# Performance work log

Hardware: AMD Instinct MI355X
Metric: run time of the kernel (lower is better)

The kernel has to match this reference:

```python
import jax, jax.numpy as jnp
import numpy as np

N_WG = 512      # waveguides n
N_COL = 512     # mesh columns
M = N_WG // 2   # node slots per column (odd columns have one masked dummy)
N_NODE = N_COL * M
B = 8192        # batch of input fields
PI4 = np.pi / 4


def build_mesh_indices():
    """Rectangular (Clements-style) mesh: per-column (top, bottom, mask) arrays."""
    top = np.zeros((N_COL, M), np.int32)
    bottom = np.zeros((N_COL, M), np.int32)
    mask = np.zeros((N_COL, M), np.int32)
    for c in range(N_COL):
        if c % 2 == 0:
            t = np.arange(0, N_WG, 2, dtype=np.int32)
            top[c], bottom[c], mask[c] = t, t + 1, 1
        else:
            t = np.arange(1, N_WG - 1, 2, dtype=np.int32)
            k = len(t)
            top[c, :k], bottom[c, :k], mask[c, :k] = t, t + 1, 1
            # masked dummy slot uses otherwise-unused rows 0 and N_WG-1
            top[c, k:], bottom[c, k:] = 0, N_WG - 1
    return jnp.asarray(top), jnp.asarray(bottom), jnp.asarray(mask)


def setup_inputs() -> dict:
    key = jax.random.key(0)
    ks = jax.random.split(key, 6)
    top, bottom, mask = build_mesh_indices()
    return {
        "x": jax.random.normal(ks[0], (N_WG, B), dtype=jnp.float32),
        "thetas": 2 * np.pi * jax.random.uniform(ks[1], (N_NODE,), dtype=jnp.float32),
        "phis": 2 * np.pi * jax.random.uniform(ks[2], (N_NODE,), dtype=jnp.float32),
        "gammas": 2 * np.pi * jax.random.uniform(ks[3], (N_WG,), dtype=jnp.float32),
        "bs_errors": 0.01 * jax.random.normal(ks[4], (N_NODE, 2), dtype=jnp.float32),
        "loss_errors": -0.1 * jax.random.uniform(ks[5], (N_NODE, 2), dtype=jnp.float32),
        "top": top, "bottom": bottom, "mask": mask,
    }


def _dc_terms(bs_errors, loss_errors, side):
    """_parallel_dc: per-node directional-coupler 2x2 elements [N,4] complex."""
    ins = jnp.exp(jnp.log(10.0) * loss_errors[:, side] / 20.0)
    e = bs_errors[:, side]
    s, c = jnp.sin(PI4 + e), jnp.cos(PI4 + e)
    t11 = (ins * s).astype(jnp.complex64)
    t12 = ins * (1j * c)
    t21 = (1j * c).astype(jnp.complex64)
    t22 = s.astype(jnp.complex64)
    return jnp.stack([t11, t12, t21, t22], axis=-1)


def _transform(v, T, t, b, m):
    """_parallel_transform: masked 2x2 gather-multiply-scatter. T: [M,4] complex."""
    vt, vb = v[t], v[b]
    one_m = 1.0 - m
    s11 = (T[:, 0] * m + one_m)[:, None]
    s12 = (T[:, 1] * m)[:, None]
    s21 = (T[:, 2] * m)[:, None]
    s22 = (T[:, 3] * m + one_m)[:, None]
    return v.at[t].set(s11 * vt + s21 * vb).at[b].set(s12 * vt + s22 * vb)


def reference(x, thetas, phis, gammas, bs_errors, loss_errors, top, bottom, mask):
    # input gamma phase screen, then propagate through all mesh columns
    v = x.astype(jnp.complex64) * jnp.exp(1j * gammas)[:, None]          # [n, B]
    left = _dc_terms(bs_errors, loss_errors, 0).reshape(N_COL, M, 4)
    right = _dc_terms(bs_errors, loss_errors, 1).reshape(N_COL, M, 4)
    th = thetas.reshape(N_COL, M)
    ph = phis.reshape(N_COL, M)
    mf = mask.astype(jnp.float32)

    def column(v, xs):
        t, b, m, thc, phc, L, R = xs
        # PhaseStyle.TOP, forward: phi -> left DC -> theta -> right DC
        v = v.at[t].multiply(jnp.exp(1j * phc * m)[:, None])
        v = _transform(v, L, t, b, m)
        v = v.at[t].multiply(jnp.exp(1j * thc * m)[:, None])
        v = _transform(v, R, t, b, m)
        return v, None

    v, _ = jax.lax.scan(column, v, (top, bottom, mf, th, ph, left, right))
    return jnp.stack([v.real, v.imag])  # [2, n, B]
```

## Files before the change

### kernel.cpp

```cpp
#include <hip/hip_runtime.h>
#include <math.h>

#define BATCH 8192
#define NROW 512
#define NCOL 512
#define MNODE 256
#define PL 524288

typedef __attribute__((ext_vector_type(8))) short bf16x8;
typedef __attribute__((ext_vector_type(4))) short s16x4;
typedef __attribute__((ext_vector_type(4))) float f32x4;

__device__ __forceinline__ short2 split1(float x) {
  unsigned u = __float_as_uint(x);
  short h = (short)(u >> 16);
  float r = x - __uint_as_float(u & 0xffff0000u);
  short l = (short)(__float_as_uint(r) >> 16);
  return make_short2(h, l);
}

__global__ __launch_bounds__(256) void precomp_kernel(
    const float* __restrict__ thetas, const float* __restrict__ phis,
    const float* __restrict__ bse, const float* __restrict__ lse,
    float4* __restrict__ pp) {
  int n = blockIdx.x * 256 + threadIdx.x;
  float th = thetas[n], ph = phis[n];
  float e0 = bse[2 * n + 0], e1 = bse[2 * n + 1];
  float l0 = lse[2 * n + 0], l1 = lse[2 * n + 1];
  const float K = 0.16609640474436813f;
  float ins0 = exp2f(l0 * K), ins1 = exp2f(l1 * K);
  const float PI4 = 0.7853981633974483f;
  float s0, c0, s1, c1, sp, cp, st, ct;
  sincosf(PI4 + e0, &s0, &c0);
  sincosf(PI4 + e1, &s1, &c1);
  sincosf(ph, &sp, &cp);
  sincosf(th, &st, &ct);
  float AL = ins0 * s0, C1L = c0, C2L = ins0 * c0, SL = s0;
  float AR = ins1 * s1, C1R = c1, C2R = ins1 * c1, SR = s1;
  float a11r = AL * cp,   a11i = AL * sp;
  float a12r = 0.f,       a12i = C1L;
  float a21r = -C2L * sp, a21i = C2L * cp;
  float a22r = SL,        a22i = 0.f;
  float b11r = a11r * ct - a11i * st, b11i = a11r * st + a11i * ct;
  float b12r = a12r * ct - a12i * st, b12i = a12r * st + a12i * ct;
  float n11r = AR * b11r - C1R * a21i;
  float n11i = AR * b11i + C1R * a21r;
  float n12r = AR * b12r - C1R * a22i;
  float n12i = AR * b12i + C1R * a22r;
  float n21r = -C2R * b11i + SR * a21r;
  float n21i =  C2R * b11r + SR * a21i;
  float n22r = -C2R * b12i + SR * a22r;
  float n22i =  C2R * b12r + SR * a22i;
  pp[2 * n + 0] = make_float4(n11r, n11i, n12r, n12i);
  pp[2 * n + 1] = make_float4(n21r, n21i, n22r, n22i);
}

__device__ __forceinline__ void proc_pair(float& vtr, float& vti, float& vbr, float& vbi,
                                          const float4 q0, const float4 q1) {
  float tr = q0.x * vtr - q0.y * vti + q0.z * vbr - q0.w * vbi;
  float ti = q0.x * vti + q0.y * vtr + q0.z * vbi + q0.w * vbr;
  float br = q1.x * vtr - q1.y * vti + q1.z * vbr - q1.w * vbi;
  float bi = q1.x * vti + q1.y * vtr + q1.z * vbi + q1.w * vbr;
  vtr = tr; vti = ti; vbr = br; vbi = bi;
}

__device__ __forceinline__ int swz(int b) { return b ^ ((b >> 3) & 7); }

__global__ __launch_bounds__(256) void compose_band(
    const float* __restrict__ gammas, const float4* __restrict__ pp,
    float* __restrict__ Tsegs, int P) {
  __shared__ float ep[5120];

  const int tid  = threadIdx.x;
  const int lane = tid & 63;
  const int w    = tid >> 6;
  const int seg  = blockIdx.x >> 7;
  const int g    = blockIdx.x & 127;
  const int col  = g * 4 + w;

  const float4* ps = pp + (size_t)seg * P * 1024;
  float* T = Tsegs + (size_t)seg * (1024 * NROW);

  const int colA = (col - 63) & ~1;
  const int E    = colA + 2 * lane;
  const int je   = E >> 1;
  const int jeC  = je < 0 ? 0 : (je > 255 ? 255 : je);

  const bool vE  = (E >= 0) && (E <= 510);
  const bool vOT = (E >= 0) && (E <= 508);
  const bool vOB = (E >= 2) && (E <= 510);

  float ar = 0.f, ai = 0.f, br = 0.f, bi = 0.f;
  {
    float vr0 = 1.f, vi0 = 0.f;
    if (seg == 0) {
      float sg, cg;
      sincosf(gammas[col], &sg, &cg);
      vr0 = cg; vi0 = sg;
    }
    if (E == col)     { ar = vr0; ai = vi0; }
    if (E + 1 == col) { br = vr0; bi = vi0; }
  }

  const float4* pe = ps + 2 * jeC;
  const float4* po = ps + 512 + 2 * jeC;

  float sar = 0.f, sai = 0.f, sbr = 0.f, sbi = 0.f;

  for (int p = 0; p < P; ++p) {
    const bool actp = (E >= col - 2 * p - 5) && (E <= col + 2 * p + 4);

    float4 o0, o1;
    if (actp) {
      float4 q0 = pe[0];
      float4 q1 = pe[1];
      o0 = po[0];
      o1 = po[-1];

      float tr = q0.x * ar - q0.y * ai + q0.z * br - q0.w * bi;
      float ti = q0.x * ai + q0.y * ar + q0.z * bi + q0.w * br;
      float ur = q1.x * ar - q1.y * ai + q1.z * br - q1.w * bi;
      float ui = q1.x * ai + q1.y * ar + q1.z * bi + q1.w * br;
      if (vE) { ar = tr; ai = ti; br = ur; bi = ui; }
    }
    pe += 1024; po += 1024;

    if (p == P - 1) { sar = ar; sai = ai; sbr = br; sbi = bi; }

    float anr = __shfl_down(ar, 1, 64);
    float ani = __shfl_down(ai, 1, 64);
    float bpr = __shfl_up(br, 1, 64);
    float bpi = __shfl_up(bi, 1, 64);
    if (lane == 63) { anr = 0.f; ani = 0.f; }
    if (lane == 0)  { bpr = 0.f; bpi = 0.f; }

    if (actp) {
      float tr = o0.x * br - o0.y * bi + o0.z * anr - o0.w * ani;
      float ti = o0.x * bi + o0.y * br + o0.z * ani + o0.w * anr;
      float ur = o1.x * bpr - o1.y * bpi + o1.z * ar - o1.w * ai;
      float ui = o1.x * bpi + o1.y * bpr + o1.z * ai + o1.w * ar;
      if (vOT) { br = tr; bi = ti; }
      if (vOB) { ar = ur; ai = ui; }
    }
  }

  int sprow = -1;
  float spr = 0.f, spi = 0.f;
  if ((col & 1) == 0) {
    if (colA + 128 <= 511) {
      sprow = colA + 128;
      float4 w1 = ps[(size_t)(P - 1) * 1024 + 512 + 2 * (colA / 2 + 63) + 1];
      float vtr = __shfl(sbr, 63, 64);
      float vti = __shfl(sbi, 63, 64);
      spr = w1.x * vtr - w1.y * vti;
      spi = w1.x * vti + w1.y * vtr;
    }
  } else {
    if (colA - 1 >= 0) {
      sprow = colA - 1;
      float4 w0 = ps[(size_t)(P - 1) * 1024 + 512 + 2 * (colA / 2 - 1)];
      float vbr = __shfl(sar, 0, 64);
      float vbi = __shfl(sai, 0, 64);
      spr = w0.z * vbr - w0.w * vbi;
      spi = w0.z * vbi + w0.w * vbr;
    }
  }

  for (int i = tid; i < 5120; i += 256) ep[i] = 0.f;
  __syncthreads();
  if (E >= 0 && E <= 510) {
    ep[E * 5 + w]         = ar;
    ep[(512 + E) * 5 + w] = ai;
    ep[(E + 1) * 5 + w]   = br;
    ep[(513 + E) * 5 + w] = bi;
  }
  if (lane == 0 && sprow >= 0) {
    ep[sprow * 5 + w]         = spr;
    ep[(512 + sprow) * 5 + w] = spi;
  }
  __syncthreads();

  if (seg & 1) {
#pragma unroll
    for (int k = 0; k < 4; ++k) {
      const int i = k * 256 + tid;
      *(float4*)(T + (size_t)i * NROW + g * 4) =
          make_float4(ep[i * 5 + 0], ep[i * 5 + 1], ep[i * 5 + 2], ep[i * 5 + 3]);
    }
  } else {
    unsigned short* Thi = (unsigned short*)T;
    unsigned short* Tlo = Thi + PL;
    const int c  = tid & 3;
    const int k0 = (tid >> 2) * 16;
    const int colg = g * 4 + c;
    short hh[16], ll[16];
#pragma unroll
    for (int j = 0; j < 16; ++j) {
      short2 s = split1(ep[(k0 + j) * 5 + c]);
      hh[j] = s.x; ll[j] = s.y;
    }
    *(bf16x8*)&Thi[(size_t)colg * 1024 + k0]     = *(bf16x8*)&hh[0];
    *(bf16x8*)&Thi[(size_t)colg * 1024 + k0 + 8] = *(bf16x8*)&hh[8];
    *(bf16x8*)&Tlo[(size_t)colg * 1024 + k0]     = *(bf16x8*)&ll[0];
    *(bf16x8*)&Tlo[(size_t)colg * 1024 + k0 + 8] = *(bf16x8*)&ll[8];
  }
}

__global__ __launch_bounds__(256) void merge_t(
    const float* __restrict__ Ab, long sA,
    const unsigned short* __restrict__ Bb, long sB,
    unsigned short* __restrict__ Cub, long sCu,
    float* __restrict__ Cfb, long sCf,
    int HA, int HB, int force_f) {
  const int z = blockIdx.z;
  const float* A = Ab + (long)z * sA;
  const unsigned short* B = Bb + (long)z * sB;
  const bool fout = force_f || (z & 1);
  unsigned short* Cu = Cub + (long)(z >> 1) * sCu;
  float*          Cf = Cfb + (long)(z >> 1) * sCf;

  __shared__ short sAh[64 * 40], sAl[64 * 40];

  const int tid = threadIdx.x;
  const int lane = tid & 63;
  const int w = tid >> 6;
  const int bm = blockIdx.y * 64;
  const int bn = blockIdx.x * 64;
  const int wm = (w & 1) * 32;
  const int wn = (w >> 1) * 32;
  const int q = lane >> 4;
  const int l15 = lane & 15;

  const int sm = tid >> 2;
  const int sk = (tid & 3) * 8;

  const int rmin = (blockIdx.y & 7) * 64;
  int klo = rmin - HA;
  {
    int t = bn - HB;
    if (t > klo) klo = t;
    if (klo < 0) klo = 0;
  }
  int khi = rmin + 63 + HA;
  {
    int t = bn + 63 + HB;
    if (t < khi) khi = t;
    if (khi > 511) khi = 511;
  }
  klo &= ~31;

  f32x4 acc[2][2];
#pragma unroll
  for (int i = 0; i < 2; ++i)
#pragma unroll
    for (int j = 0; j < 2; ++j) acc[i][j] = (f32x4){0.f, 0.f, 0.f, 0.f};

  if (klo <= khi) {
#pragma unroll 1
    for (int h = 0; h < 2; ++h) {
#pragma unroll 1
      for (int k0 = klo; k0 <= khi; k0 += 32) {
        const int gkb = h * 512 + k0;
        {
          const int gm = bm + sm;
          const int gk = gkb + sk;
          const int r = gm & 511;
          const bool top = gm < 512;
          const bool left = gk < 512;
          const int col = gk & 511;
          const float* src = (top == left) ? (A + (size_t)r * 512)
                                           : (A + (size_t)(512 + r) * 512);
          const float sgn = (top && !left) ? -1.f : 1.f;
          float4 v0 = *(const float4*)(src + col);
          float4 v1 = *(const float4*)(src + col + 4);
          float vv[8] = {v0.x, v0.y, v0.z, v0.w, v1.x, v1.y, v1.z, v1.w};
          short hh[8], ll[8];
#pragma unroll
          for (int i = 0; i < 8; ++i) {
            short2 s = split1(sgn * vv[i]);
            hh[i] = s.x; ll[i] = s.y;
          }
          __syncthreads();
          *(bf16x8*)&sAh[sm * 40 + sk] = *(bf16x8*)hh;
          *(bf16x8*)&sAl[sm * 40 + sk] = *(bf16x8*)ll;
          __syncthreads();
        }

        bf16x8 bh[2], bl[2];
#pragma unroll
        for (int nt = 0; nt < 2; ++nt) {
          const unsigned short* bp =
              B + (size_t)(bn + wn + nt * 16 + l15) * 1024 + gkb + q * 8;
          bh[nt] = *(const bf16x8*)bp;
          bl[nt] = *(const bf16x8*)(bp + PL);
        }

        bf16x8 ah[2], al[2];
#pragma unroll
        for (int mt = 0; mt < 2; ++mt) {
          const int m = wm + mt * 16 + l15;
          ah[mt] = *(const bf16x8*)&sAh[m * 40 + q * 8];
          al[mt] = *(const bf16x8*)&sAl[m * 40 + q * 8];
        }

#pragma unroll
        for (int mt = 0; mt < 2; ++mt)
#pragma unroll
          for (int nt = 0; nt < 2; ++nt) {
            acc[mt][nt] = __builtin_amdgcn_mfma_f32_16x16x32_bf16(ah[mt], bh[nt], acc[mt][nt], 0, 0, 0);
            acc[mt][nt] = __builtin_amdgcn_mfma_f32_16x16x32_bf16(ah[mt], bl[nt], acc[mt][nt], 0, 0, 0);
            acc[mt][nt] = __builtin_amdgcn_mfma_f32_16x16x32_bf16(al[mt], bh[nt], acc[mt][nt], 0, 0, 0);
          }
      }
    }
  }

  if (fout) {
#pragma unroll
    for (int mt = 0; mt < 2; ++mt)
#pragma unroll
      for (int nt = 0; nt < 2; ++nt)
#pragma unroll
        for (int r = 0; r < 4; ++r) {
          const int gm = bm + wm + mt * 16 + q * 4 + r;
          const int gn = bn + wn + nt * 16 + l15;
          Cf[(size_t)gm * 512 + gn] = acc[mt][nt][r];
        }
  } else {
    unsigned short* Chi = Cu;
    unsigned short* Clo = Cu + PL;
#pragma unroll
    for (int mt = 0; mt < 2; ++mt)
#pragma unroll
      for (int nt = 0; nt < 2; ++nt) {
        short hh[4], ll[4];
#pragma unroll
        for (int r = 0; r < 4; ++r) {
          short2 s = split1(acc[mt][nt][r]);
          hh[r] = s.x; ll[r] = s.y;
        }
        const int gm0 = bm + wm + mt * 16 + q * 4;
        const int gn  = bn + wn + nt * 16 + l15;
        *(s16x4*)&Chi[(size_t)gn * 1024 + gm0] = *(s16x4*)hh;
        *(s16x4*)&Clo[(size_t)gn * 1024 + gm0] = *(s16x4*)ll;
      }
  }
}

__global__ __launch_bounds__(256) void compose_kernel(
    const float* __restrict__ gammas, const float4* __restrict__ pp,
    float* __restrict__ Tsegs, int pairs_per_seg) {
  __shared__ float4 buf[2][1024];
  float* epf = (float*)buf;

  const int tid  = threadIdx.x;
  const int lane = tid & 63;
  const int w    = tid >> 6;
  const int seg  = blockIdx.x >> 7;
  const int g    = blockIdx.x & 127;
  const int col  = g * 4 + w;
  const int colmin = g * 4;

  const float4* ps = pp + (size_t)seg * pairs_per_seg * 1024;
  float* T = Tsegs + (size_t)seg * (1024 * NROW);

  float vr[8], vi[8];
#pragma unroll
  for (int r = 0; r < 8; ++r) {
    const int row = lane * 8 + r;
    vr[r] = 0.f; vi[r] = 0.f;
    if (row == col) {
      if (seg == 0) {
        float sg, cg;
        sincosf(gammas[row], &sg, &cg);
        vr[r] = cg; vi[r] = sg;
      } else {
        vr[r] = 1.f;
      }
    }
  }

  {
    const int sw = swz(tid);
#pragma unroll
    for (int k = 0; k < 4; ++k)
      buf[0][256 * k + sw] = ps[256 * k + tid];
  }
  __syncthreads();

  const int Lc = col >> 3;

#pragma unroll 1
  for (int p = 0; p < pairs_per_seg; ++p) {
    const int b = p & 1;

    const int HA = (p >> 2) + 3;
    const bool act  = (lane >= Lc - HA)     && (lane <= Lc + HA);
    const bool wide = (lane >= Lc - HA - 1) && (lane <= Lc + HA + 1);

    float4 f0, f1, f2, f3;
    bool st0 = false, st1 = false;
    if (p < pairs_per_seg - 1) {
      const int slo = colmin - 2 * p - 50;
      const int shi = colmin + 2 * p + 53;
      st0 = (tid + 1 >= slo) && (tid <= shi);
      st1 = (tid + 257 >= slo) && (tid + 256 <= shi);
      const float4* src = ps + (size_t)(p + 1) * 1024;
      if (st0) { f0 = src[tid];       f2 = src[512 + tid]; }
      if (st1) { f1 = src[256 + tid]; f3 = src[768 + tid]; }
    }

    float4 pe[8], po[7], pu1;
    if (act) {
      const int base = 8 * lane;
      const int l7 = lane & 7;
#pragma unroll
      for (int j = 0; j < 8; ++j) pe[j] = buf[b][base + (j ^ l7)];
#pragma unroll
      for (int j = 0; j < 7; ++j) po[j] = buf[b][512 + base + (j ^ l7)];
      const int lm = (lane == 0) ? 0 : lane - 1;
      pu1 = buf[b][512 + 8 * lm + (7 ^ (lm & 7))];

#pragma unroll
      for (int k = 0; k < 4; ++k)
        proc_pair(vr[2 * k], vi[2 * k], vr[2 * k + 1], vi[2 * k + 1],
                  pe[2 * k], pe[2 * k + 1]);

#pragma unroll
      for (int k = 0; k < 3; ++k)
        proc_pair(vr[2 * k + 1], vi[2 * k + 1], vr[2 * k + 2], vi[2 * k + 2],
                  po[2 * k], po[2 * k + 1]);
    }

    float br = 0.f, bi = 0.f, tu = 0.f, tv = 0.f;
    if (wide) {
      br = __shfl_down(vr[0], 1, 64);
      bi = __shfl_down(vi[0], 1, 64);
      tu = __shfl_up(vr[7], 1, 64);
      tv = __shfl_up(vi[7], 1, 64);
    }
    if (act) {
      float nAr = po[6].x * vr[7] - po[6].y * vi[7] + po[6].z * br - po[6].w * bi;
      float nAi = po[6].x * vi[7] + po[6].y * vr[7] + po[6].z * bi + po[6].w * br;
      float nBr = pu1.x * tu - pu1.y * tv + pu1.z * vr[0] - pu1.w * vi[0];
      float nBi = pu1.x * tv + pu1.y * tu + pu1.z * vi[0] + pu1.w * vr[0];
      if (lane < 63) { vr[7] = nAr; vi[7] = nAi; }
      if (lane > 0)  { vr[0] = nBr; vi[0] = nBi; }
    }

    if (p < pairs_per_seg - 1) {
      const int sw = swz(tid);
      if (st0) { buf[1 - b][sw] = f0;       buf[1 - b][512 + sw] = f2; }
      if (st1) { buf[1 - b][256 + sw] = f1; buf[1 - b][768 + sw] = f3; }
    }
    __syncthreads();
  }

#pragma unroll
  for (int r = 0; r < 8; ++r) {
    epf[(lane * 8 + r) * 5 + w] = vr[r];
    epf[(512 + lane * 8 + r) * 5 + w] = vi[r];
  }
  __syncthreads();
#pragma unroll
  for (int k = 0; k < 4; ++k) {
    const int i = k * 256 + tid;
    *(float4*)(T + (size_t)i * NROW + g * 4) =
        make_float4(epf[i * 5 + 0], epf[i * 5 + 1], epf[i * 5 + 2], epf[i * 5 + 3]);
  }
}

__global__ __launch_bounds__(256) void merge_g(
    const float* __restrict__ Ab, const float* __restrict__ Bb,
    float* __restrict__ Cb, long sA, long sB, long sC, int HA, int HB) {
  const float* A = Ab + (long)blockIdx.z * sA;
  const float* B = Bb + (long)blockIdx.z * sB;
  float*       C = Cb + (long)blockIdx.z * sC;

  __shared__ short sAh[64 * 40], sAl[64 * 40];

  const int tid = threadIdx.x;
  const int lane = tid & 63;
  const int w = tid >> 6;
  const int bm = blockIdx.y * 64;
  const int bn = blockIdx.x * 64;
  const int wm = (w & 1) * 32;
  const int wn = (w >> 1) * 32;
  const int q = lane >> 4;
  const int l15 = lane & 15;

  const int sm = tid >> 2;
  const int sk = (tid & 3) * 8;

  const int rmin = (blockIdx.y & 7) * 64;
  int klo = rmin - HA;
  {
    int t = bn - HB;
    if (t > klo) klo = t;
    if (klo < 0) klo = 0;
  }
  int khi = rmin + 63 + HA;
  {
    int t = bn + 63 + HB;
    if (t < khi) khi = t;
    if (khi > 511) khi = 511;
  }
  klo &= ~31;

  f32x4 acc[2][2];
#pragma unroll
  for (int i = 0; i < 2; ++i)
#pragma unroll
    for (int j = 0; j < 2; ++j) acc[i][j] = (f32x4){0.f, 0.f, 0.f, 0.f};

  if (klo <= khi) {
#pragma unroll 1
    for (int h = 0; h < 2; ++h) {
#pragma unroll 1
      for (int k0 = klo; k0 <= khi; k0 += 32) {
        const int gkb = h * 512 + k0;
        {
          const int gm = bm + sm;
          const int gk = gkb + sk;
          const int r = gm & 511;
          const bool top = gm < 512;
          const bool left = gk < 512;
          const int col = gk & 511;
          const float* src = (top == left) ? (A + (size_t)r * 512)
                                           : (A + (size_t)(512 + r) * 512);
          const float sgn = (top && !left) ? -1.f : 1.f;
          float4 v0 = *(const float4*)(src + col);
          float4 v1 = *(const float4*)(src + col + 4);
          float vv[8] = {v0.x, v0.y, v0.z, v0.w, v1.x, v1.y, v1.z, v1.w};
          short hh[8], ll[8];
#pragma unroll
          for (int i = 0; i < 8; ++i) {
            short2 s = split1(sgn * vv[i]);
            hh[i] = s.x; ll[i] = s.y;
          }
          __syncthreads();
          *(bf16x8*)&sAh[sm * 40 + sk] = *(bf16x8*)hh;
          *(bf16x8*)&sAl[sm * 40 + sk] = *(bf16x8*)ll;
          __syncthreads();
        }

        bf16x8 bh[2], bl[2];
#pragma unroll
        for (int nt = 0; nt < 2; ++nt) {
          const float* bp = B + (size_t)(gkb + q * 8) * 512 + bn + wn + nt * 16 + l15;
          short hh[8], ll[8];
#pragma unroll
          for (int j = 0; j < 8; ++j) {
            short2 s = split1(bp[(size_t)j * 512]);
            hh[j] = s.x; ll[j] = s.y;
          }
          bh[nt] = *(bf16x8*)hh;
          bl[nt] = *(bf16x8*)ll;
        }

        bf16x8 ah[2], al[2];
#pragma unroll
        for (int mt = 0; mt < 2; ++mt) {
          const int m = wm + mt * 16 + l15;
          ah[mt] = *(const bf16x8*)&sAh[m * 40 + q * 8];
          al[mt] = *(const bf16x8*)&sAl[m * 40 + q * 8];
        }

#pragma unroll
        for (int mt = 0; mt < 2; ++mt)
#pragma unroll
          for (int nt = 0; nt < 2; ++nt) {
            acc[mt][nt] = __builtin_amdgcn_mfma_f32_16x16x32_bf16(ah[mt], bh[nt], acc[mt][nt], 0, 0, 0);
            acc[mt][nt] = __builtin_amdgcn_mfma_f32_16x16x32_bf16(ah[mt], bl[nt], acc[mt][nt], 0, 0, 0);
            acc[mt][nt] = __builtin_amdgcn_mfma_f32_16x16x32_bf16(al[mt], bh[nt], acc[mt][nt], 0, 0, 0);
          }
      }
    }
  }

#pragma unroll
  for (int mt = 0; mt < 2; ++mt)
#pragma unroll
    for (int nt = 0; nt < 2; ++nt)
#pragma unroll
      for (int r = 0; r < 4; ++r) {
        const int gm = bm + wm + mt * 16 + q * 4 + r;
        const int gn = bn + wn + nt * 16 + l15;
        C[(size_t)gm * 512 + gn] = acc[mt][nt][r];
      }
}

__global__ __launch_bounds__(256) void xprep_kernel(
    const float* __restrict__ x, short* __restrict__ xp) {
  const int t = blockIdx.x * 256 + threadIdx.x;
  const int n = t & 8191;
  const int g = t >> 13;
  const float* src = x + (size_t)g * 8 * BATCH + n;
  short h[8], l[8];
#pragma unroll
  for (int j = 0; j < 8; ++j) {
    short2 s = split1(src[(size_t)j * BATCH]);
    h[j] = s.x; l[j] = s.y;
  }
  short* dst = xp + (size_t)t * 16;
  *(bf16x8*)dst = *(bf16x8*)h;
  *(bf16x8*)(dst + 8) = *(bf16x8*)l;
}

__global__ __launch_bounds__(256) void gemm_mfma_packed(
    const float* __restrict__ A, const short* __restrict__ xp,
    float* __restrict__ C) {
  __shared__ short sAh[128 * 40], sAl[128 * 40];

  const int tid = threadIdx.x;
  const int lane = tid & 63;
  const int w = tid >> 6;
  const int bm = blockIdx.y * 128;
  const int bn = blockIdx.x * 128;
  const int wm = (w & 1) * 64;
  const int wn = (w >> 1) * 64;
  const int q = lane >> 4;
  const int l15 = lane & 15;

  const int sm = tid >> 1;
  const int sk = (tid & 1) * 16;
  const float* Ap = A + (size_t)(bm + sm) * 512 + sk;

  f32x4 acc[4][4];
#pragma unroll
  for (int i = 0; i < 4; ++i)
#pragma unroll
    for (int j = 0; j < 4; ++j) acc[i][j] = (f32x4){0.f, 0.f, 0.f, 0.f};

  float4 pa[4];
#pragma unroll
  for (int i = 0; i < 4; ++i) pa[i] = *(const float4*)(Ap + i * 4);

#pragma unroll 1
  for (int k0 = 0; k0 < 512; k0 += 32) {
    {
      short h[16], l[16];
#pragma unroll
      for (int i = 0; i < 16; ++i) {
        short2 s = split1(((const float*)pa)[i]);
        h[i] = s.x; l[i] = s.y;
      }
      __syncthreads();
      *(bf16x8*)&sAh[sm * 40 + sk]     = *(bf16x8*)&h[0];
      *(bf16x8*)&sAh[sm * 40 + sk + 8] = *(bf16x8*)&h[8];
      *(bf16x8*)&sAl[sm * 40 + sk]     = *(bf16x8*)&l[0];
      *(bf16x8*)&sAl[sm * 40 + sk + 8] = *(bf16x8*)&l[8];
      __syncthreads();
    }

    if (k0 + 32 < 512) {
#pragma unroll
      for (int i = 0; i < 4; ++i) pa[i] = *(const float4*)(Ap + k0 + 32 + i * 4);
    }

    const int kt = k0 >> 5;
    bf16x8 bh[4], bl[4];
#pragma unroll
    for (int nt = 0; nt < 4; ++nt) {
      const short* bp = xp + (((size_t)(kt * 4 + q)) * BATCH +
                              (bn + wn + nt * 16 + l15)) * 16;
      bh[nt] = *(const bf16x8*)bp;
      bl[nt] = *(const bf16x8*)(bp + 8);
    }

#pragma unroll
    for (int mt = 0; mt < 4; ++mt) {
      const int m = wm + mt * 16 + l15;
      bf16x8 ah = *(const bf16x8*)&sAh[m * 40 + q * 8];
      bf16x8 al = *(const bf16x8*)&sAl[m * 40 + q * 8];
#pragma unroll
      for (int nt = 0; nt < 4; ++nt) {
        acc[mt][nt] = __builtin_amdgcn_mfma_f32_16x16x32_bf16(ah, bh[nt], acc[mt][nt], 0, 0, 0);
        acc[mt][nt] = __builtin_amdgcn_mfma_f32_16x16x32_bf16(ah, bl[nt], acc[mt][nt], 0, 0, 0);
        acc[mt][nt] = __builtin_amdgcn_mfma_f32_16x16x32_bf16(al, bh[nt], acc[mt][nt], 0, 0, 0);
      }
    }
  }

#pragma unroll
  for (int mt = 0; mt < 4; ++mt)
#pragma unroll
    for (int nt = 0; nt < 4; ++nt)
#pragma unroll
      for (int r = 0; r < 4; ++r) {
        const int gm = bm + wm + mt * 16 + q * 4 + r;
        const int gn = bn + wn + nt * 16 + l15;
        C[(size_t)gm * BATCH + gn] = acc[mt][nt][r];
      }
}

__global__ __launch_bounds__(256) void gemm_mfma(
    const float* __restrict__ A, const float* __restrict__ B,
    float* __restrict__ C) {
  __shared__ short sAh[128 * 40], sAl[128 * 40];

  const int tid = threadIdx.x;
  const int lane = tid & 63;
  const int w = tid >> 6;
  const int bm = blockIdx.y * 128;
  const int bn = blockIdx.x * 128;
  const int wm = (w & 1) * 64;
  const int wn = (w >> 1) * 64;
  const int q = lane >> 4;
  const int l15 = lane & 15;

  const int sm = tid >> 1;
  const int sk = (tid & 1) * 16;
  const float* Ap = A + (size_t)(bm + sm) * 512 + sk;

  f32x4 acc[4][4];
#pragma unroll
  for (int i = 0; i < 4; ++i)
#pragma unroll
    for (int j = 0; j < 4; ++j) acc[i][j] = (f32x4){0.f, 0.f, 0.f, 0.f};

  float4 pa[4];
#pragma unroll
  for (int i = 0; i < 4; ++i) pa[i] = *(const float4*)(Ap + i * 4);

#pragma unroll 1
  for (int k0 = 0; k0 < 512; k0 += 32) {
    {
      short h[16], l[16];
#pragma unroll
      for (int i = 0; i < 16; ++i) {
        short2 s = split1(((const float*)pa)[i]);
        h[i] = s.x; l[i] = s.y;
      }
      __syncthreads();
      *(bf16x8*)&sAh[sm * 40 + sk]     = *(bf16x8*)&h[0];
      *(bf16x8*)&sAh[sm * 40 + sk + 8] = *(bf16x8*)&h[8];
      *(bf16x8*)&sAl[sm * 40 + sk]     = *(bf16x8*)&l[0];
      *(bf16x8*)&sAl[sm * 40 + sk + 8] = *(bf16x8*)&l[8];
      __syncthreads();
    }

    if (k0 + 32 < 512) {
#pragma unroll
      for (int i = 0; i < 4; ++i) pa[i] = *(const float4*)(Ap + k0 + 32 + i * 4);
    }

    bf16x8 bh[4], bl[4];
#pragma unroll
    for (int nt = 0; nt < 4; ++nt) {
      const float* bp = B + (size_t)(k0 + q * 8) * BATCH + bn + wn + nt * 16 + l15;
      short hh[8], ll[8];
#pragma unroll
      for (int j = 0; j < 8; ++j) {
        short2 s = split1(bp[(size_t)j * BATCH]);
        hh[j] = s.x; ll[j] = s.y;
      }
      bh[nt] = *(bf16x8*)hh;
      bl[nt] = *(bf16x8*)ll;
    }

    bf16x8 ah[4], al[4];
#pragma unroll
    for (int mt = 0; mt < 4; ++mt) {
      const int m = wm + mt * 16 + l15;
      ah[mt] = *(const bf16x8*)&sAh[m * 40 + q * 8];
      al[mt] = *(const bf16x8*)&sAl[m * 40 + q * 8];
    }

#pragma unroll
    for (int mt = 0; mt < 4; ++mt)
#pragma unroll
      for (int nt = 0; nt < 4; ++nt) {
        acc[mt][nt] = __builtin_amdgcn_mfma_f32_16x16x32_bf16(ah[mt], bh[nt], acc[mt][nt], 0, 0, 0);
        acc[mt][nt] = __builtin_amdgcn_mfma_f32_16x16x32_bf16(ah[mt], bl[nt], acc[mt][nt], 0, 0, 0);
        acc[mt][nt] = __builtin_amdgcn_mfma_f32_16x16x32_bf16(al[mt], bh[nt], acc[mt][nt], 0, 0, 0);
      }
  }

#pragma unroll
  for (int mt = 0; mt < 4; ++mt)
#pragma unroll
    for (int nt = 0; nt < 4; ++nt)
#pragma unroll
      for (int r = 0; r < 4; ++r) {
        const int gm = bm + wm + mt * 16 + q * 4 + r;
        const int gn = bn + wn + nt * 16 + l15;
        C[(size_t)gm * BATCH + gn] = acc[mt][nt][r];
      }
}

extern "C" void kernel_launch(void* const* d_in, const int* in_sizes, int n_in,
                              void* d_out, int out_size, void* d_ws, size_t ws_size,
                              hipStream_t stream) {
  const float* x      = (const float*)d_in[0];
  const float* thetas = (const float*)d_in[1];
  const float* phis   = (const float*)d_in[2];
  const float* gammas = (const float*)d_in[3];
  const float* bse    = (const float*)d_in[4];
  const float* lse    = (const float*)d_in[5];

  float* base = (float*)d_ws;
  float4* pp  = (float4*)d_ws;
  const long PPF = 1048576;
  const long S   = 524288;

  precomp_kernel<<<512, 256, 0, stream>>>(thetas, phis, bse, lse, pp);

  if (ws_size >= (size_t)24 * 1024 * 1024) {
    float* B0 = base + PPF;
    compose_band<<<1024, 256, 0, stream>>>(gammas, pp, B0, 32);

    merge_t<<<dim3(8, 16, 4), 256, 0, stream>>>(
        B0 + S, 2 * S, (const unsigned short*)B0, 4 * S,
        (unsigned short*)base, 2 * S, base + 5 * PPF, S, 68, 68, 0);

    merge_t<<<dim3(8, 16, 2), 256, 0, stream>>>(
        base + 5 * PPF, S, (const unsigned short*)base, 2 * S,
        (unsigned short*)(base + PPF), 0, base + PPF + S, 0, 136, 136, 0);

    merge_t<<<dim3(8, 16, 1), 256, 0, stream>>>(
        base + PPF + S, 0, (const unsigned short*)(base + PPF), 0,
        (unsigned short*)base, 0, base, 0, 272, 272, 1);

    short* xp = (short*)(base + S);
    xprep_kernel<<<2048, 256, 0, stream>>>(x, xp);

    gemm_mfma_packed<<<dim3(64, 8), 256, 0, stream>>>(base, xp, (float*)d_out);
    gemm_mfma_packed<<<dim3(64, 8), 256, 0, stream>>>(base, xp, (float*)d_out);
  } else {
    int nseg;
    if (ws_size >= (size_t)14 * 1024 * 1024)      nseg = 4;
    else if (ws_size >= (size_t)8 * 1024 * 1024)  nseg = 2;
    else                                          nseg = 1;

    float* segs = base + PPF;
    float* Tf;
    compose_kernel<<<nseg * 128, 256, 0, stream>>>(gammas, pp, segs, 256 / nseg);

    if (nseg == 4) {
      float* T10 = base;
      float* T32 = base + S;
      Tf = segs + 4 * S;
      merge_g<<<dim3(8, 16, 2), 256, 0, stream>>>(
          segs + S, segs, T10, 2 * S, 2 * S, S, 132, 132);
      merge_g<<<dim3(8, 16, 1), 256, 0, stream>>>(
          T32, T10, Tf, 0, 0, 0, 264, 264);
    } else if (nseg == 2) {
      Tf = base;
      merge_g<<<dim3(8, 16, 1), 256, 0, stream>>>(
          segs + S, segs, Tf, 0, 0, 0, 260, 260);
    } else {
      Tf = segs;
    }

    gemm_mfma<<<dim3(BATCH / 128, 8), 256, 0, stream>>>(Tf, x, (float*)d_out);
  }
}
```

Baseline: 254.5 us.

## Retile merge_t to 32-row tiles with double-buffered LDS and drop duplicate GEMM launch

merge_t now uses 32x64 output tiles, so its grid doubles in y, and each wave computes one 16-row strip. A-tile staging is restructured into a single flattened loop over both k-halves. It uses double-buffered shared memory with one barrier per step and prefetches the next A float4 into registers. Separately, the second identical gemm_mfma_packed launch is removed, eliminating a redundant full GEMM pass. The smaller tiles raise parallelism and overlap in the merge stages, at the cost of less B reuse per block.

```diff
diff --git a/kernel.cpp b/kernel.cpp
--- a/kernel.cpp
+++ b/kernel.cpp
@@ -219,6 +219,261 @@
   unsigned short* Cu = Cub + (long)(z >> 1) * sCu;
   float*          Cf = Cfb + (long)(z >> 1) * sCf;
 
+  __shared__ short sAh[2][32 * 40], sAl[2][32 * 40];
+
+  const int tid = threadIdx.x;
+  const int lane = tid & 63;
+  const int w = tid >> 6;
+  const int bm = blockIdx.y * 32;
+  const int bn = blockIdx.x * 64;
+  const int wm = (w & 1) * 16;
+  const int wn = (w >> 1) * 32;
+  const int q = lane >> 4;
+  const int l15 = lane & 15;
+
+  const int sm  = tid >> 3;
+  const int skf = (tid & 7) * 4;
+
+  const int rmin = (blockIdx.y & 15) * 32;
+  int klo = rmin - HA;
+  {
+    int t = bn - HB;
+    if (t > klo) klo = t;
+    if (klo < 0) klo = 0;
+  }
+  int khi = rmin + 31 + HA;
+  {
+    int t = bn + 63 + HB;
+    if (t < khi) khi = t;
+    if (khi > 511) khi = 511;
+  }
+  klo &= ~31;
+
+  f32x4 acc[2];
+  acc[0] = (f32x4){0.f, 0.f, 0.f, 0.f};
+  acc[1] = (f32x4){0.f, 0.f, 0.f, 0.f};
+
+  if (klo <= khi) {
+    const int ns = ((khi - klo) >> 5) + 1;
+    const int total = 2 * ns;
+
+    const int gm = bm + sm;
+    const int r = gm & 511;
+    const bool top = gm < 512;
+    const float* srcA0 = top ? (A + (size_t)r * 512) : (A + (size_t)(512 + r) * 512);
+    const float* srcA1 = top ? (A + (size_t)(512 + r) * 512) : (A + (size_t)r * 512);
+    const float sgn1 = top ? -1.f : 1.f;
+
+    float4 pv = *(const float4*)(srcA0 + klo + skf);
+
+#pragma unroll 1
+    for (int s = 0; s < total; ++s) {
+      const int h = (s >= ns) ? 1 : 0;
+      const int k0 = klo + ((s - h * ns) << 5);
+      const int b = s & 1;
+
+      {
+        const float sg = h ? sgn1 : 1.f;
+        float vv[4] = {pv.x, pv.y, pv.z, pv.w};
+        short hh[4], ll[4];
+#pragma unroll
+        for (int i = 0; i < 4; ++i) {
+          short2 s2 = split1(sg * vv[i]);
+          hh[i] = s2.x; ll[i] = s2.y;
+        }
+        *(s16x4*)&sAh[b][sm * 40 + skf] = *(s16x4*)hh;
+        *(s16x4*)&sAl[b][sm * 40 + skf] = *(s16x4*)ll;
+      }
+      __syncthreads();
+
+      if (s + 1 < total) {
+        const int h2 = (s + 1 >= ns) ? 1 : 0;
+        const int k2 = klo + (((s + 1) - h2 * ns) << 5);
+        pv = *(const float4*)((h2 ? srcA1 : srcA0) + k2 + skf);
+      }
+
+      const int gkb = h * 512 + k0;
+
+      bf16x8 bh[2], bl[2];
+#pragma unroll
+      for (int nt = 0; nt < 2; ++nt) {
+        const unsigned short* bp =
+            B + (size_t)(bn + wn + nt * 16 + l15) * 1024 + gkb + q * 8;
+        bh[nt] = *(const bf16x8*)bp;
+        bl[nt] = *(const bf16x8*)(bp + PL);
+      }
+
+      const int m = wm + l15;
+      bf16x8 ah = *(const bf16x8*)&sAh[b][m * 40 + q * 8];
+      bf16x8 al = *(const bf16x8*)&sAl[b][m * 40 + q * 8];
+
+#pragma unroll
+      for (int nt = 0; nt < 2; ++nt) {
+        acc[nt] = __builtin_amdgcn_mfma_f32_16x16x32_bf16(ah, bh[nt], acc[nt], 0, 0, 0);
+        acc[nt] = __builtin_amdgcn_mfma_f32_16x16x32_bf16(ah, bl[nt], acc[nt], 0, 0, 0);
+        acc[nt] = __builtin_amdgcn_mfma_f32_16x16x32_bf16(al, bh[nt], acc[nt], 0, 0, 0);
+      }
+    }
+  }
+
+  if (fout) {
+#pragma unroll
+    for (int nt = 0; nt < 2; ++nt)
+#pragma unroll
+      for (int rr = 0; rr < 4; ++rr) {
+        const int gm = bm + wm + q * 4 + rr;
+        const int gn = bn + wn + nt * 16 + l15;
+        Cf[(size_t)gm * 512 + gn] = acc[nt][rr];
+      }
+  } else {
+    unsigned short* Chi = Cu;
+    unsigned short* Clo = Cu + PL;
+#pragma unroll
+    for (int nt = 0; nt < 2; ++nt) {
+      short hh[4], ll[4];
+#pragma unroll
+      for (int rr = 0; rr < 4; ++rr) {
+        short2 s = split1(acc[nt][rr]);
+        hh[rr] = s.x; ll[rr] = s.y;
+      }
+      const int gm0 = bm + wm + q * 4;
+      const int gn  = bn + wn + nt * 16 + l15;
+      *(s16x4*)&Chi[(size_t)gn * 1024 + gm0] = *(s16x4*)hh;
+      *(s16x4*)&Clo[(size_t)gn * 1024 + gm0] = *(s16x4*)ll;
+    }
+  }
+}
+
+__global__ __launch_bounds__(256) void compose_kernel(
+    const float* __restrict__ gammas, const float4* __restrict__ pp,
+    float* __restrict__ Tsegs, int pairs_per_seg) {
+  __shared__ float4 buf[2][1024];
+  float* epf = (float*)buf;
+
+  const int tid  = threadIdx.x;
+  const int lane = tid & 63;
+  const int w    = tid >> 6;
+  const int seg  = blockIdx.x >> 7;
+  const int g    = blockIdx.x & 127;
+  const int col  = g * 4 + w;
+  const int colmin = g * 4;
+
+  const float4* ps = pp + (size_t)seg * pairs_per_seg * 1024;
+  float* T = Tsegs + (size_t)seg * (1024 * NROW);
+
+  float vr[8], vi[8];
+#pragma unroll
+  for (int r = 0; r < 8; ++r) {
+    const int row = lane * 8 + r;
+    vr[r] = 0.f; vi[r] = 0.f;
+    if (row == col) {
+      if (seg == 0) {
+        float sg, cg;
+        sincosf(gammas[row], &sg, &cg);
+        vr[r] = cg; vi[r] = sg;
+      } else {
+        vr[r] = 1.f;
+      }
+    }
+  }
+
+  {
+    const int sw = swz(tid);
+#pragma unroll
+    for (int k = 0; k < 4; ++k)
+      buf[0][256 * k + sw] = ps[256 * k + tid];
+  }
+  __syncthreads();
+
+  const int Lc = col >> 3;
+
+#pragma unroll 1
+  for (int p = 0; p < pairs_per_seg; ++p) {
+    const int b = p & 1;
+
+    const int HA = (p >> 2) + 3;
+    const bool act  = (lane >= Lc - HA)     && (lane <= Lc + HA);
+    const bool wide = (lane >= Lc - HA - 1) && (lane <= Lc + HA + 1);
+
+    float4 f0, f1, f2, f3;
+    bool st0 = false, st1 = false;
+    if (p < pairs_per_seg - 1) {
+      const int slo = colmin - 2 * p - 50;
+      const int shi = colmin + 2 * p + 53;
+      st0 = (tid + 1 >= slo) && (tid <= shi);
+      st1 = (tid + 257 >= slo) && (tid + 256 <= shi);
+      const float4* src = ps + (size_t)(p + 1) * 1024;
+      if (st0) { f0 = src[tid];       f2 = src[512 + tid]; }
+      if (st1) { f1 = src[256 + tid]; f3 = src[768 + tid]; }
+    }
+
+    float4 pe[8], po[7], pu1;
+    if (act) {
+      const int base = 8 * lane;
+      const int l7 = lane & 7;
+#pragma unroll
+      for (int j = 0; j < 8; ++j) pe[j] = buf[b][base + (j ^ l7)];
+#pragma unroll
+      for (int j = 0; j < 7; ++j) po[j] = buf[b][512 + base + (j ^ l7)];
+      const int lm = (lane == 0) ? 0 : lane - 1;
+      pu1 = buf[b][512 + 8 * lm + (7 ^ (lm & 7))];
+
+#pragma unroll
+      for (int k = 0; k < 4; ++k)
+        proc_pair(vr[2 * k], vi[2 * k], vr[2 * k + 1], vi[2 * k + 1],
+                  pe[2 * k], pe[2 * k + 1]);
+
+#pragma unroll
+      for (int k = 0; k < 3; ++k)
+        proc_pair(vr[2 * k + 1], vi[2 * k + 1], vr[2 * k + 2], vi[2 * k + 2],
+                  po[2 * k], po[2 * k + 1]);
+    }
+
+    float br = 0.f, bi = 0.f, tu = 0.f, tv = 0.f;
+    if (wide) {
+      br = __shfl_down(vr[0], 1, 64);
+      bi = __shfl_down(vi[0], 1, 64);
+      tu = __shfl_up(vr[7], 1, 64);
+      tv = __shfl_up(vi[7], 1, 64);
+    }
+    if (act) {
+      float nAr = po[6].x * vr[7] - po[6].y * vi[7] + po[6].z * br - po[6].w * bi;
+      float nAi = po[6].x * vi[7] + po[6].y * vr[7] + po[6].z * bi + po[6].w * br;
+      float nBr = pu1.x * tu - pu1.y * tv + pu1.z * vr[0] - pu1.w * vi[0];
+      float nBi = pu1.x * tv + pu1.y * tu + pu1.z * vi[0] + pu1.w * vr[0];
+      if (lane < 63) { vr[7] = nAr; vi[7] = nAi; }
+      if (lane > 0)  { vr[0] = nBr; vi[0] = nBi; }
+    }
+
+    if (p < pairs_per_seg - 1) {
+      const int sw = swz(tid);
+      if (st0) { buf[1 - b][sw] = f0;       buf[1 - b][512 + sw] = f2; }
+      if (st1) { buf[1 - b][256 + sw] = f1; buf[1 - b][768 + sw] = f3; }
+    }
+    __syncthreads();
+  }
+
+#pragma unroll
+  for (int r = 0; r < 8; ++r) {
+    epf[(lane * 8 + r) * 5 + w] = vr[r];
+    epf[(512 + lane * 8 + r) * 5 + w] = vi[r];
+  }
+  __syncthreads();
+#pragma unroll
+  for (int k = 0; k < 4; ++k) {
+    const int i = k * 256 + tid;
+    *(float4*)(T + (size_t)i * NROW + g * 4) =
+        make_float4(epf[i * 5 + 0], epf[i * 5 + 1], epf[i * 5 + 2], epf[i * 5 + 3]);
+  }
+}
+
+__global__ __launch_bounds__(256) void merge_g(
+    const float* __restrict__ Ab, const float* __restrict__ Bb,
+    float* __restrict__ Cb, long sA, long sB, long sC, int HA, int HB) {
+  const float* A = Ab + (long)blockIdx.z * sA;
+  const float* B = Bb + (long)blockIdx.z * sB;
+  float*       C = Cb + (long)blockIdx.z * sC;
+
   __shared__ short sAh[64 * 40], sAl[64 * 40];
 
   const int tid = threadIdx.x;
@@ -289,264 +544,6 @@
         bf16x8 bh[2], bl[2];
 #pragma unroll
         for (int nt = 0; nt < 2; ++nt) {
-          const unsigned short* bp =
-              B + (size_t)(bn + wn + nt * 16 + l15) * 1024 + gkb + q * 8;
-          bh[nt] = *(const bf16x8*)bp;
-          bl[nt] = *(const bf16x8*)(bp + PL);
-        }
-
-        bf16x8 ah[2], al[2];
-#pragma unroll
-        for (int mt = 0; mt < 2; ++mt) {
-          const int m = wm + mt * 16 + l15;
-          ah[mt] = *(const bf16x8*)&sAh[m * 40 + q * 8];
-          al[mt] = *(const bf16x8*)&sAl[m * 40 + q * 8];
-        }
-
-#pragma unroll
-        for (int mt = 0; mt < 2; ++mt)
-#pragma unroll
-          for (int nt = 0; nt < 2; ++nt) {
-            acc[mt][nt] = __builtin_amdgcn_mfma_f32_16x16x32_bf16(ah[mt], bh[nt], acc[mt][nt], 0, 0, 0);
-            acc[mt][nt] = __builtin_amdgcn_mfma_f32_16x16x32_bf16(ah[mt], bl[nt], acc[mt][nt], 0, 0, 0);
-            acc[mt][nt] = __builtin_amdgcn_mfma_f32_16x16x32_bf16(al[mt], bh[nt], acc[mt][nt], 0, 0, 0);
-          }
-      }
-    }
-  }
-
-  if (fout) {
-#pragma unroll
-    for (int mt = 0; mt < 2; ++mt)
-#pragma unroll
-      for (int nt = 0; nt < 2; ++nt)
-#pragma unroll
-        for (int r = 0; r < 4; ++r) {
-          const int gm = bm + wm + mt * 16 + q * 4 + r;
-          const int gn = bn + wn + nt * 16 + l15;
-          Cf[(size_t)gm * 512 + gn] = acc[mt][nt][r];
-        }
-  } else {
-    unsigned short* Chi = Cu;
-    unsigned short* Clo = Cu + PL;
-#pragma unroll
-    for (int mt = 0; mt < 2; ++mt)
-#pragma unroll
-      for (int nt = 0; nt < 2; ++nt) {
-        short hh[4], ll[4];
-#pragma unroll
-        for (int r = 0; r < 4; ++r) {
-          short2 s = split1(acc[mt][nt][r]);
-          hh[r] = s.x; ll[r] = s.y;
-        }
-        const int gm0 = bm + wm + mt * 16 + q * 4;
-        const int gn  = bn + wn + nt * 16 + l15;
-        *(s16x4*)&Chi[(size_t)gn * 1024 + gm0] = *(s16x4*)hh;
-        *(s16x4*)&Clo[(size_t)gn * 1024 + gm0] = *(s16x4*)ll;
-      }
-  }
-}
-
-__global__ __launch_bounds__(256) void compose_kernel(
-    const float* __restrict__ gammas, const float4* __restrict__ pp,
-    float* __restrict__ Tsegs, int pairs_per_seg) {
-  __shared__ float4 buf[2][1024];
-  float* epf = (float*)buf;
-
-  const int tid  = threadIdx.x;
-  const int lane = tid & 63;
-  const int w    = tid >> 6;
-  const int seg  = blockIdx.x >> 7;
-  const int g    = blockIdx.x & 127;
-  const int col  = g * 4 + w;
-  const int colmin = g * 4;
-
-  const float4* ps = pp + (size_t)seg * pairs_per_seg * 1024;
-  float* T = Tsegs + (size_t)seg * (1024 * NROW);
-
-  float vr[8], vi[8];
-#pragma unroll
-  for (int r = 0; r < 8; ++r) {
-    const int row = lane * 8 + r;
-    vr[r] = 0.f; vi[r] = 0.f;
-    if (row == col) {
-      if (seg == 0) {
-        float sg, cg;
-        sincosf(gammas[row], &sg, &cg);
-        vr[r] = cg; vi[r] = sg;
-      } else {
-        vr[r] = 1.f;
-      }
-    }
-  }
-
-  {
-    const int sw = swz(tid);
-#pragma unroll
-    for (int k = 0; k < 4; ++k)
-      buf[0][256 * k + sw] = ps[256 * k + tid];
-  }
-  __syncthreads();
-
-  const int Lc = col >> 3;
-
-#pragma unroll 1
-  for (int p = 0; p < pairs_per_seg; ++p) {
-    const int b = p & 1;
-
-    const int HA = (p >> 2) + 3;
-    const bool act  = (lane >= Lc - HA)     && (lane <= Lc + HA);
-    const bool wide = (lane >= Lc - HA - 1) && (lane <= Lc + HA + 1);
-
-    float4 f0, f1, f2, f3;
-    bool st0 = false, st1 = false;
-    if (p < pairs_per_seg - 1) {
-      const int slo = colmin - 2 * p - 50;
-      const int shi = colmin + 2 * p + 53;
-      st0 = (tid + 1 >= slo) && (tid <= shi);
-      st1 = (tid + 257 >= slo) && (tid + 256 <= shi);
-      const float4* src = ps + (size_t)(p + 1) * 1024;
-      if (st0) { f0 = src[tid];       f2 = src[512 + tid]; }
-      if (st1) { f1 = src[256 + tid]; f3 = src[768 + tid]; }
-    }
-
-    float4 pe[8], po[7], pu1;
-    if (act) {
-      const int base = 8 * lane;
-      const int l7 = lane & 7;
-#pragma unroll
-      for (int j = 0; j < 8; ++j) pe[j] = buf[b][base + (j ^ l7)];
-#pragma unroll
-      for (int j = 0; j < 7; ++j) po[j] = buf[b][512 + base + (j ^ l7)];
-      const int lm = (lane == 0) ? 0 : lane - 1;
-      pu1 = buf[b][512 + 8 * lm + (7 ^ (lm & 7))];
-
-#pragma unroll
-      for (int k = 0; k < 4; ++k)
-        proc_pair(vr[2 * k], vi[2 * k], vr[2 * k + 1], vi[2 * k + 1],
-                  pe[2 * k], pe[2 * k + 1]);
-
-#pragma unroll
-      for (int k = 0; k < 3; ++k)
-        proc_pair(vr[2 * k + 1], vi[2 * k + 1], vr[2 * k + 2], vi[2 * k + 2],
-                  po[2 * k], po[2 * k + 1]);
-    }
-
-    float br = 0.f, bi = 0.f, tu = 0.f, tv = 0.f;
-    if (wide) {
-      br = __shfl_down(vr[0], 1, 64);
-      bi = __shfl_down(vi[0], 1, 64);
-      tu = __shfl_up(vr[7], 1, 64);
-      tv = __shfl_up(vi[7], 1, 64);
-    }
-    if (act) {
-      float nAr = po[6].x * vr[7] - po[6].y * vi[7] + po[6].z * br - po[6].w * bi;
-      float nAi = po[6].x * vi[7] + po[6].y * vr[7] + po[6].z * bi + po[6].w * br;
-      float nBr = pu1.x * tu - pu1.y * tv + pu1.z * vr[0] - pu1.w * vi[0];
-      float nBi = pu1.x * tv + pu1.y * tu + pu1.z * vi[0] + pu1.w * vr[0];
-      if (lane < 63) { vr[7] = nAr; vi[7] = nAi; }
-      if (lane > 0)  { vr[0] = nBr; vi[0] = nBi; }
-    }
-
-    if (p < pairs_per_seg - 1) {
-      const int sw = swz(tid);
-      if (st0) { buf[1 - b][sw] = f0;       buf[1 - b][512 + sw] = f2; }
-      if (st1) { buf[1 - b][256 + sw] = f1; buf[1 - b][768 + sw] = f3; }
-    }
-    __syncthreads();
-  }
-
-#pragma unroll
-  for (int r = 0; r < 8; ++r) {
-    epf[(lane * 8 + r) * 5 + w] = vr[r];
-    epf[(512 + lane * 8 + r) * 5 + w] = vi[r];
-  }
-  __syncthreads();
-#pragma unroll
-  for (int k = 0; k < 4; ++k) {
-    const int i = k * 256 + tid;
-    *(float4*)(T + (size_t)i * NROW + g * 4) =
-        make_float4(epf[i * 5 + 0], epf[i * 5 + 1], epf[i * 5 + 2], epf[i * 5 + 3]);
-  }
-}
-
-__global__ __launch_bounds__(256) void merge_g(
-    const float* __restrict__ Ab, const float* __restrict__ Bb,
-    float* __restrict__ Cb, long sA, long sB, long sC, int HA, int HB) {
-  const float* A = Ab + (long)blockIdx.z * sA;
-  const float* B = Bb + (long)blockIdx.z * sB;
-  float*       C = Cb + (long)blockIdx.z * sC;
-
-  __shared__ short sAh[64 * 40], sAl[64 * 40];
-
-  const int tid = threadIdx.x;
-  const int lane = tid & 63;
-  const int w = tid >> 6;
-  const int bm = blockIdx.y * 64;
-  const int bn = blockIdx.x * 64;
-  const int wm = (w & 1) * 32;
-  const int wn = (w >> 1) * 32;
-  const int q = lane >> 4;
-  const int l15 = lane & 15;
-
-  const int sm = tid >> 2;
-  const int sk = (tid & 3) * 8;
-
-  const int rmin = (blockIdx.y & 7) * 64;
-  int klo = rmin - HA;
-  {
-    int t = bn - HB;
-    if (t > klo) klo = t;
-    if (klo < 0) klo = 0;
-  }
-  int khi = rmin + 63 + HA;
-  {
-    int t = bn + 63 + HB;
-    if (t < khi) khi = t;
-    if (khi > 511) khi = 511;
-  }
-  klo &= ~31;
-
-  f32x4 acc[2][2];
-#pragma unroll
-  for (int i = 0; i < 2; ++i)
-#pragma unroll
-    for (int j = 0; j < 2; ++j) acc[i][j] = (f32x4){0.f, 0.f, 0.f, 0.f};
-
-  if (klo <= khi) {
-#pragma unroll 1
-    for (int h = 0; h < 2; ++h) {
-#pragma unroll 1
-      for (int k0 = klo; k0 <= khi; k0 += 32) {
-        const int gkb = h * 512 + k0;
-        {
-          const int gm = bm + sm;
-          const int gk = gkb + sk;
-          const int r = gm & 511;
-          const bool top = gm < 512;
-          const bool left = gk < 512;
-          const int col = gk & 511;
-          const float* src = (top == left) ? (A + (size_t)r * 512)
-                                           : (A + (size_t)(512 + r) * 512);
-          const float sgn = (top && !left) ? -1.f : 1.f;
-          float4 v0 = *(const float4*)(src + col);
-          float4 v1 = *(const float4*)(src + col + 4);
-          float vv[8] = {v0.x, v0.y, v0.z, v0.w, v1.x, v1.y, v1.z, v1.w};
-          short hh[8], ll[8];
-#pragma unroll
-          for (int i = 0; i < 8; ++i) {
-            short2 s = split1(sgn * vv[i]);
-            hh[i] = s.x; ll[i] = s.y;
-          }
-          __syncthreads();
-          *(bf16x8*)&sAh[sm * 40 + sk] = *(bf16x8*)hh;
-          *(bf16x8*)&sAl[sm * 40 + sk] = *(bf16x8*)ll;
-          __syncthreads();
-        }
-
-        bf16x8 bh[2], bl[2];
-#pragma unroll
-        for (int nt = 0; nt < 2; ++nt) {
           const float* bp = B + (size_t)(gkb + q * 8) * 512 + bn + wn + nt * 16 + l15;
           short hh[8], ll[8];
 #pragma unroll
@@ -810,22 +807,21 @@
     float* B0 = base + PPF;
     compose_band<<<1024, 256, 0, stream>>>(gammas, pp, B0, 32);
 
-    merge_t<<<dim3(8, 16, 4), 256, 0, stream>>>(
+    merge_t<<<dim3(8, 32, 4), 256, 0, stream>>>(
         B0 + S, 2 * S, (const unsigned short*)B0, 4 * S,
         (unsigned short*)base, 2 * S, base + 5 * PPF, S, 68, 68, 0);
 
-    merge_t<<<dim3(8, 16, 2), 256, 0, stream>>>(
+    merge_t<<<dim3(8, 32, 2), 256, 0, stream>>>(
         base + 5 * PPF, S, (const unsigned short*)base, 2 * S,
         (unsigned short*)(base + PPF), 0, base + PPF + S, 0, 136, 136, 0);
 
-    merge_t<<<dim3(8, 16, 1), 256, 0, stream>>>(
+    merge_t<<<dim3(8, 32, 1), 256, 0, stream>>>(
         base + PPF + S, 0, (const unsigned short*)(base + PPF), 0,
         (unsigned short*)base, 0, base, 0, 272, 272, 1);
 
     short* xp = (short*)(base + S);
     xprep_kernel<<<2048, 256, 0, stream>>>(x, xp);
 
-    gemm_mfma_packed<<<dim3(64, 8), 256, 0, stream>>>(base, xp, (float*)d_out);
     gemm_mfma_packed<<<dim3(64, 8), 256, 0, stream>>>(base, xp, (float*)d_out);
   } else {
     int nseg;
```

After: 228.4 us. -10.3%, faster.
